# Kernel optimization log

Measured on AMD Instinct MI355X. Metric: run time of the kernel, lower is better.

## Reference

```python
import jax, jax.numpy as jnp
import numpy as np

N = 10000      # nodes (docstring: dense mode intended for <=10k nodes)
D_IN = 64      # in_dim
D_OUT = 64     # out_dim


def setup_inputs() -> dict:
    key = jax.random.key(0)
    kH, kA1, kA2, kA3, kW1, kW2, kW3 = jax.random.split(key, 7)
    H = jax.random.normal(kH, (N, D_IN), dtype=jnp.float32)
    # Dense normalized adjacency per edge type (values in [0,1), as in A_norm)
    A_r1 = jax.random.uniform(kA1, (N, N), dtype=jnp.float32)
    A_r2 = jax.random.uniform(kA2, (N, N), dtype=jnp.float32)
    A_r3 = jax.random.uniform(kA3, (N, N), dtype=jnp.float32)
    # Xavier-uniform init for type-specific linear weights [out_dim, in_dim]
    limit = float(np.sqrt(6.0 / (D_IN + D_OUT)))
    W1 = jax.random.uniform(kW1, (D_OUT, D_IN), dtype=jnp.float32, minval=-limit, maxval=limit)
    W2 = jax.random.uniform(kW2, (D_OUT, D_IN), dtype=jnp.float32, minval=-limit, maxval=limit)
    W3 = jax.random.uniform(kW3, (D_OUT, D_IN), dtype=jnp.float32, minval=-limit, maxval=limit)
    bias = jnp.zeros((D_OUT,), dtype=jnp.float32)
    return {"H": H, "A_r1": A_r1, "A_r2": A_r2, "A_r3": A_r3,
            "W1": W1, "W2": W2, "W3": W3, "bias": bias}


def reference(H, A_r1, A_r2, A_r3, W1, W2, W3, bias):
    # h_v = sum_r W_r @ (sum_u A_r[v,u] * h_u) + b  (no activation in forward)
    out = bias  # broadcasts to [N, D_OUT]
    for A_r, W_r in ((A_r1, W1), (A_r2, W2), (A_r3, W3)):
        msg = A_r @ H                      # [N, D_IN] neighbor aggregation
        out = out + msg @ W_r.T            # [N, D_OUT] type-specific projection
    return out
```

## Files before the change

kernel.cpp:

```cpp
#include <hip/hip_runtime.h>

static constexpr int NN = 10000;
static constexpr int DD = 64;
static constexpr int KP = 10240;
static constexpr int BK = 128;
static constexpr int SPLITS = 4;
static constexpr int KC = KP / SPLITS;
static constexpr int ITERS = KC / BK;
static constexpr int BM = 64;

typedef __attribute__((ext_vector_type(4))) float f32x4;
typedef __attribute__((ext_vector_type(8))) short s16x8;
typedef __attribute__((ext_vector_type(4))) unsigned short u16x4;

__device__ __forceinline__ unsigned short f2bf(float f) {
  unsigned u = __float_as_uint(f);
  return (unsigned short)((u + 0x7fffu + ((u >> 16) & 1u)) >> 16);
}

__device__ __forceinline__ void g2l16(const void* g, void* l) {
  __builtin_amdgcn_global_load_lds((const __attribute__((address_space(1))) unsigned int*)g,
                                   (__attribute__((address_space(3))) unsigned int*)l, 16, 0, 0);
}

__global__ void prep_kernel(const float* __restrict__ H,
                            const float* __restrict__ W1,
                            const float* __restrict__ W2,
                            const float* __restrict__ W3,
                            unsigned short* __restrict__ mt) {
  const int r = blockIdx.y;
  const float* W = (r == 0) ? W1 : (r == 1) ? W2 : W3;
  const int wave = threadIdx.x >> 6;
  const int lane = threadIdx.x & 63;
  f32x4 wr[16];
#pragma unroll
  for (int i = 0; i < 16; ++i) wr[i] = *(const f32x4*)&W[lane * 64 + i * 4];
  unsigned short* orow = mt + ((size_t)r * 64 + lane) * KP;
  const int kbase = blockIdx.x * 128 + wave * 32;
  for (int i = 0; i < 32; ++i) {
    const int k = kbase + i;
    if (k < NN) {
      float s = 0.f;
#pragma unroll
      for (int j = 0; j < 16; ++j) {
        f32x4 h = *(const f32x4*)&H[(size_t)k * 64 + j * 4];
        s += h[0] * wr[j][0] + h[1] * wr[j][1] + h[2] * wr[j][2] + h[3] * wr[j][3];
      }
      orow[k] = f2bf(s);
    } else {
      orow[k] = 0;
    }
  }
}

__global__ void init_out_kernel(const float* __restrict__ bias, float* __restrict__ out) {
  const int i = blockIdx.x * 256 + threadIdx.x;
  if (i < NN * DD) out[i] = bias[i & 63];
}

__global__ __launch_bounds__(256, 2) void gcn_main(const float* __restrict__ A1,
                                                   const float* __restrict__ A2,
                                                   const float* __restrict__ A3,
                                                   const unsigned short* __restrict__ mt,
                                                   float* __restrict__ out) {
  __shared__ __align__(1024) unsigned short mldsM[2][64][128];
  __shared__ __align__(1024) unsigned short mldsA[2][64][128];

  const int r = blockIdx.z;
  const int s = blockIdx.y;
  const float* A = (r == 0) ? A1 : (r == 1) ? A2 : A3;
  const unsigned short* mtr = mt + (size_t)r * 64 * KP;

  const int wave = threadIdx.x >> 6;
  const int lane = threadIdx.x & 63;
  const int l15 = lane & 15;
  const int lhi = lane >> 4;
  const int l31 = lane & 31;
  const int lh5 = lane >> 5;
  const int v0 = blockIdx.x * BM;
  const int k0 = s * KC;

  const float* rowPtr[8];
  int wOff[8];
#pragma unroll
  for (int j = 0; j < 8; ++j) {
    const int rloc = wave * 16 + 2 * j + lh5;
    int vr = v0 + rloc; if (vr > NN - 1) vr = NN - 1;
    rowPtr[j] = A + (size_t)vr * NN;
    wOff[j] = rloc * 256 + (((l31 >> 1) ^ (rloc & 15)) * 16) + (lane & 1) * 8;
  }
  int rOffA[4], rOffM[4][4];
#pragma unroll
  for (int kk = 0; kk < 4; ++kk) {
    rOffA[kk] = (wave * 16 + l15) * 256 + (((kk * 4 + lhi) ^ l15) * 16);
#pragma unroll
    for (int dt = 0; dt < 4; ++dt)
      rOffM[kk][dt] = (dt * 16 + l15) * 256 + (((kk * 4 + lhi) ^ l15) * 16);
  }

  f32x4 acc[4] = {{0.f,0.f,0.f,0.f},{0.f,0.f,0.f,0.f},{0.f,0.f,0.f,0.f},{0.f,0.f,0.f,0.f}};
  f32x4 ar[8];

  auto stageM = [&](int t, int buf) {
    const int kb = k0 + t * BK;
#pragma unroll
    for (int j = 0; j < 4; ++j) {
      const int row16 = 4 * j + (lane >> 4);
      const int rowabs = wave * 16 + row16;
      const unsigned short* src = mtr + (size_t)rowabs * KP + kb + (((lane & 15) ^ row16) << 3);
      g2l16(src, &mldsM[buf][wave * 16 + 4 * j][0]);
    }
  };

  auto issueA = [&](int kb) {
    int koff = kb + l31 * 4;
    if (koff > NN - 4) koff = NN - 4;
    const float* p0 = rowPtr[0] + koff; const float* p1 = rowPtr[1] + koff;
    const float* p2 = rowPtr[2] + koff; const float* p3 = rowPtr[3] + koff;
    const float* p4 = rowPtr[4] + koff; const float* p5 = rowPtr[5] + koff;
    const float* p6 = rowPtr[6] + koff; const float* p7 = rowPtr[7] + koff;
    asm volatile(
      "global_load_dwordx4 %0, %8, off\n\t"
      "global_load_dwordx4 %1, %9, off\n\t"
      "global_load_dwordx4 %2, %10, off\n\t"
      "global_load_dwordx4 %3, %11, off\n\t"
      "global_load_dwordx4 %4, %12, off\n\t"
      "global_load_dwordx4 %5, %13, off\n\t"
      "global_load_dwordx4 %6, %14, off\n\t"
      "global_load_dwordx4 %7, %15, off"
      : "=&v"(ar[0]), "=&v"(ar[1]), "=&v"(ar[2]), "=&v"(ar[3]),
        "=&v"(ar[4]), "=&v"(ar[5]), "=&v"(ar[6]), "=&v"(ar[7])
      : "v"(p0), "v"(p1), "v"(p2), "v"(p3), "v"(p4), "v"(p5), "v"(p6), "v"(p7));
  };

  auto cvtWrite = [&](int buf, int kb) {
    if (kb + BK > NN) {
      if (kb + l31 * 4 > NN - 4) {
#pragma unroll
        for (int j = 0; j < 8; ++j) ar[j] = (f32x4){0.f, 0.f, 0.f, 0.f};
      }
    }
    char* base = (char*)&mldsA[buf][0][0];
#pragma unroll
    for (int j = 0; j < 8; ++j) {
      u16x4 c;
      c[0] = f2bf(ar[j][0]); c[1] = f2bf(ar[j][1]);
      c[2] = f2bf(ar[j][2]); c[3] = f2bf(ar[j][3]);
      *(u16x4*)(base + wOff[j]) = c;
    }
  };

  issueA(k0);
  __builtin_amdgcn_sched_barrier(0);
  stageM(0, 0);
  __builtin_amdgcn_sched_barrier(0);
  asm volatile("s_waitcnt vmcnt(4)");
  __builtin_amdgcn_sched_barrier(0);
  cvtWrite(0, k0);
  __builtin_amdgcn_sched_barrier(0);
  asm volatile("s_waitcnt vmcnt(0)");
  __builtin_amdgcn_sched_barrier(0);
  __builtin_amdgcn_s_barrier();

  for (int t = 0; t < ITERS; ++t) {
    const int buf = t & 1;
    const int tn = (t + 1 < ITERS) ? t + 1 : t;
    const int kbn = k0 + tn * BK;
    issueA(kbn);
    __builtin_amdgcn_sched_barrier(0);
    stageM(tn, buf ^ 1);
    __builtin_amdgcn_sched_barrier(0);
    {
      const char* aBase = (const char*)&mldsA[buf][0][0];
      const char* mBase = (const char*)&mldsM[buf][0][0];
#pragma unroll
      for (int kk = 0; kk < 4; ++kk) {
        s16x8 a = *(const s16x8*)(aBase + rOffA[kk]);
#pragma unroll
        for (int dt = 0; dt < 4; ++dt) {
          s16x8 b = *(const s16x8*)(mBase + rOffM[kk][dt]);
          acc[dt] = __builtin_amdgcn_mfma_f32_16x16x32_bf16(a, b, acc[dt], 0, 0, 0);
        }
      }
    }
    __builtin_amdgcn_sched_barrier(0);
    asm volatile("s_waitcnt vmcnt(4)");
    __builtin_amdgcn_sched_barrier(0);
    cvtWrite(buf ^ 1, kbn);
    __builtin_amdgcn_sched_barrier(0);
    asm volatile("s_waitcnt vmcnt(0)");
    __builtin_amdgcn_sched_barrier(0);
    __builtin_amdgcn_s_barrier();
  }

#pragma unroll
  for (int dt = 0; dt < 4; ++dt) {
    const int d = dt * 16 + l15;
#pragma unroll
    for (int i = 0; i < 4; ++i) {
      const int v = v0 + wave * 16 + lhi * 4 + i;
      if (v < NN) atomicAdd(&out[(size_t)v * DD + d], acc[dt][i]);
    }
  }
}

extern "C" void kernel_launch(void* const* d_in, const int* in_sizes, int n_in,
                              void* d_out, int out_size, void* d_ws, size_t ws_size,
                              hipStream_t stream) {
  const float* H    = (const float*)d_in[0];
  const float* A1   = (const float*)d_in[1];
  const float* A2   = (const float*)d_in[2];
  const float* A3   = (const float*)d_in[3];
  const float* W1   = (const float*)d_in[4];
  const float* W2   = (const float*)d_in[5];
  const float* W3   = (const float*)d_in[6];
  const float* bias = (const float*)d_in[7];
  float* out = (float*)d_out;
  unsigned short* mt = (unsigned short*)d_ws;

  prep_kernel<<<dim3(KP / 128, 3), 256, 0, stream>>>(H, W1, W2, W3, mt);
  init_out_kernel<<<dim3((NN * DD + 255) / 256), 256, 0, stream>>>(bias, out);
  gcn_main<<<dim3((NN + BM - 1) / BM, SPLITS, 3), 256, 0, stream>>>(A1, A2, A3, mt, out);
}
```

Measured before the change: 293.3 us.

## Add alternate direct-to-LDS fp32 A staging path for half the K-splits

Result: no change. 291.3 us (-0.7%).

```diff
diff --git a/kernel.cpp b/kernel.cpp
--- a/kernel.cpp
+++ b/kernel.cpp
@@ -3,10 +3,7 @@
 static constexpr int NN = 10000;
 static constexpr int DD = 64;
 static constexpr int KP = 10240;
-static constexpr int BK = 128;
-static constexpr int SPLITS = 4;
-static constexpr int KC = KP / SPLITS;
-static constexpr int ITERS = KC / BK;
+static constexpr int KC = 2560;
 static constexpr int BM = 64;
 
 typedef __attribute__((ext_vector_type(4))) float f32x4;
@@ -63,11 +60,10 @@
                                                    const float* __restrict__ A3,
                                                    const unsigned short* __restrict__ mt,
                                                    float* __restrict__ out) {
-  __shared__ __align__(1024) unsigned short mldsM[2][64][128];
-  __shared__ __align__(1024) unsigned short mldsA[2][64][128];
+  __shared__ __align__(1024) char smem[65536];
 
   const int r = blockIdx.z;
-  const int s = blockIdx.y;
+  const int sy = blockIdx.y;
   const float* A = (r == 0) ? A1 : (r == 1) ? A2 : A3;
   const unsigned short* mtr = mt + (size_t)r * 64 * KP;
 
@@ -75,122 +71,204 @@
   const int lane = threadIdx.x & 63;
   const int l15 = lane & 15;
   const int lhi = lane >> 4;
-  const int l31 = lane & 31;
-  const int lh5 = lane >> 5;
   const int v0 = blockIdx.x * BM;
-  const int k0 = s * KC;
-
-  const float* rowPtr[8];
-  int wOff[8];
-#pragma unroll
-  for (int j = 0; j < 8; ++j) {
-    const int rloc = wave * 16 + 2 * j + lh5;
-    int vr = v0 + rloc; if (vr > NN - 1) vr = NN - 1;
-    rowPtr[j] = A + (size_t)vr * NN;
-    wOff[j] = rloc * 256 + (((l31 >> 1) ^ (rloc & 15)) * 16) + (lane & 1) * 8;
-  }
-  int rOffA[4], rOffM[4][4];
-#pragma unroll
-  for (int kk = 0; kk < 4; ++kk) {
-    rOffA[kk] = (wave * 16 + l15) * 256 + (((kk * 4 + lhi) ^ l15) * 16);
-#pragma unroll
-    for (int dt = 0; dt < 4; ++dt)
-      rOffM[kk][dt] = (dt * 16 + l15) * 256 + (((kk * 4 + lhi) ^ l15) * 16);
-  }
+  const int k0 = sy * KC;
 
   f32x4 acc[4] = {{0.f,0.f,0.f,0.f},{0.f,0.f,0.f,0.f},{0.f,0.f,0.f,0.f},{0.f,0.f,0.f,0.f}};
-  f32x4 ar[8];
-
-  auto stageM = [&](int t, int buf) {
-    const int kb = k0 + t * BK;
-#pragma unroll
-    for (int j = 0; j < 4; ++j) {
-      const int row16 = 4 * j + (lane >> 4);
-      const int rowabs = wave * 16 + row16;
-      const unsigned short* src = mtr + (size_t)rowabs * KP + kb + (((lane & 15) ^ row16) << 3);
-      g2l16(src, &mldsM[buf][wave * 16 + 4 * j][0]);
-    }
-  };
-
-  auto issueA = [&](int kb) {
-    int koff = kb + l31 * 4;
-    if (koff > NN - 4) koff = NN - 4;
-    const float* p0 = rowPtr[0] + koff; const float* p1 = rowPtr[1] + koff;
-    const float* p2 = rowPtr[2] + koff; const float* p3 = rowPtr[3] + koff;
-    const float* p4 = rowPtr[4] + koff; const float* p5 = rowPtr[5] + koff;
-    const float* p6 = rowPtr[6] + koff; const float* p7 = rowPtr[7] + koff;
-    asm volatile(
-      "global_load_dwordx4 %0, %8, off\n\t"
-      "global_load_dwordx4 %1, %9, off\n\t"
-      "global_load_dwordx4 %2, %10, off\n\t"
-      "global_load_dwordx4 %3, %11, off\n\t"
-      "global_load_dwordx4 %4, %12, off\n\t"
-      "global_load_dwordx4 %5, %13, off\n\t"
-      "global_load_dwordx4 %6, %14, off\n\t"
-      "global_load_dwordx4 %7, %15, off"
-      : "=&v"(ar[0]), "=&v"(ar[1]), "=&v"(ar[2]), "=&v"(ar[3]),
-        "=&v"(ar[4]), "=&v"(ar[5]), "=&v"(ar[6]), "=&v"(ar[7])
-      : "v"(p0), "v"(p1), "v"(p2), "v"(p3), "v"(p4), "v"(p5), "v"(p6), "v"(p7));
-  };
-
-  auto cvtWrite = [&](int buf, int kb) {
-    if (kb + BK > NN) {
-      if (kb + l31 * 4 > NN - 4) {
-#pragma unroll
-        for (int j = 0; j < 8; ++j) ar[j] = (f32x4){0.f, 0.f, 0.f, 0.f};
-      }
-    }
-    char* base = (char*)&mldsA[buf][0][0];
+
+  if (sy < 2) {
+    constexpr int BK = 128, ITERS = 20;
+    auto mldsM = (unsigned short (*)[64][128])(smem);
+    auto mldsA = (unsigned short (*)[64][128])(smem + 32768);
+
+    const int l31 = lane & 31;
+    const int lh5 = lane >> 5;
+
+    const float* rowPtr[8];
+    int wOff[8];
 #pragma unroll
     for (int j = 0; j < 8; ++j) {
-      u16x4 c;
-      c[0] = f2bf(ar[j][0]); c[1] = f2bf(ar[j][1]);
-      c[2] = f2bf(ar[j][2]); c[3] = f2bf(ar[j][3]);
-      *(u16x4*)(base + wOff[j]) = c;
-    }
-  };
-
-  issueA(k0);
-  __builtin_amdgcn_sched_barrier(0);
-  stageM(0, 0);
-  __builtin_amdgcn_sched_barrier(0);
-  asm volatile("s_waitcnt vmcnt(4)");
-  __builtin_amdgcn_sched_barrier(0);
-  cvtWrite(0, k0);
-  __builtin_amdgcn_sched_barrier(0);
-  asm volatile("s_waitcnt vmcnt(0)");
-  __builtin_amdgcn_sched_barrier(0);
-  __builtin_amdgcn_s_barrier();
-
-  for (int t = 0; t < ITERS; ++t) {
-    const int buf = t & 1;
-    const int tn = (t + 1 < ITERS) ? t + 1 : t;
-    const int kbn = k0 + tn * BK;
-    issueA(kbn);
-    __builtin_amdgcn_sched_barrier(0);
-    stageM(tn, buf ^ 1);
-    __builtin_amdgcn_sched_barrier(0);
-    {
-      const char* aBase = (const char*)&mldsA[buf][0][0];
-      const char* mBase = (const char*)&mldsM[buf][0][0];
-#pragma unroll
-      for (int kk = 0; kk < 4; ++kk) {
-        s16x8 a = *(const s16x8*)(aBase + rOffA[kk]);
+      const int rloc = wave * 16 + 2 * j + lh5;
+      int vr = v0 + rloc; if (vr > NN - 1) vr = NN - 1;
+      rowPtr[j] = A + (size_t)vr * NN;
+      wOff[j] = rloc * 256 + (((l31 >> 1) ^ (rloc & 15)) * 16) + (lane & 1) * 8;
+    }
+    int rOffA[4], rOffM[4][4];
+#pragma unroll
+    for (int kk = 0; kk < 4; ++kk) {
+      rOffA[kk] = (wave * 16 + l15) * 256 + (((kk * 4 + lhi) ^ l15) * 16);
+#pragma unroll
+      for (int dt = 0; dt < 4; ++dt)
+        rOffM[kk][dt] = (dt * 16 + l15) * 256 + (((kk * 4 + lhi) ^ l15) * 16);
+    }
+
+    f32x4 ar[8];
+
+    auto stageM = [&](int t, int buf) {
+      const int kb = k0 + t * BK;
+#pragma unroll
+      for (int j = 0; j < 4; ++j) {
+        const int row16 = 4 * j + (lane >> 4);
+        const int rowabs = wave * 16 + row16;
+        const unsigned short* src = mtr + (size_t)rowabs * KP + kb + (((lane & 15) ^ row16) << 3);
+        g2l16(src, &mldsM[buf][wave * 16 + 4 * j][0]);
+      }
+    };
+    auto issueA = [&](int kb) {
+      int koff = kb + l31 * 4;
+      if (koff > NN - 4) koff = NN - 4;
+      const float* p0 = rowPtr[0] + koff; const float* p1 = rowPtr[1] + koff;
+      const float* p2 = rowPtr[2] + koff; const float* p3 = rowPtr[3] + koff;
+      const float* p4 = rowPtr[4] + koff; const float* p5 = rowPtr[5] + koff;
+      const float* p6 = rowPtr[6] + koff; const float* p7 = rowPtr[7] + koff;
+      asm volatile(
+        "global_load_dwordx4 %0, %8, off\n\t"
+        "global_load_dwordx4 %1, %9, off\n\t"
+        "global_load_dwordx4 %2, %10, off\n\t"
+        "global_load_dwordx4 %3, %11, off\n\t"
+        "global_load_dwordx4 %4, %12, off\n\t"
+        "global_load_dwordx4 %5, %13, off\n\t"
+        "global_load_dwordx4 %6, %14, off\n\t"
+        "global_load_dwordx4 %7, %15, off"
+        : "=&v"(ar[0]), "=&v"(ar[1]), "=&v"(ar[2]), "=&v"(ar[3]),
+          "=&v"(ar[4]), "=&v"(ar[5]), "=&v"(ar[6]), "=&v"(ar[7])
+        : "v"(p0), "v"(p1), "v"(p2), "v"(p3), "v"(p4), "v"(p5), "v"(p6), "v"(p7));
+    };
+    auto cvtWrite = [&](int buf, int kb) {
+      if (kb + BK > NN) {
+        if (kb + l31 * 4 > NN - 4) {
+#pragma unroll
+          for (int j = 0; j < 8; ++j) ar[j] = (f32x4){0.f, 0.f, 0.f, 0.f};
+        }
+      }
+      char* base = (char*)&mldsA[0][0][0] + buf * 32768 / 2;
+#pragma unroll
+      for (int j = 0; j < 8; ++j) {
+        u16x4 c;
+        c[0] = f2bf(ar[j][0]); c[1] = f2bf(ar[j][1]);
+        c[2] = f2bf(ar[j][2]); c[3] = f2bf(ar[j][3]);
+        *(u16x4*)(base + wOff[j]) = c;
+      }
+    };
+
+    issueA(k0);
+    __builtin_amdgcn_sched_barrier(0);
+    stageM(0, 0);
+    __builtin_amdgcn_sched_barrier(0);
+    asm volatile("s_waitcnt vmcnt(4)");
+    __builtin_amdgcn_sched_barrier(0);
+    cvtWrite(0, k0);
+    __builtin_amdgcn_sched_barrier(0);
+    asm volatile("s_waitcnt vmcnt(0)");
+    __builtin_amdgcn_sched_barrier(0);
+    __builtin_amdgcn_s_barrier();
+
+    for (int t = 0; t < ITERS; ++t) {
+      const int buf = t & 1;
+      const int tn = (t + 1 < ITERS) ? t + 1 : t;
+      const int kbn = k0 + tn * BK;
+      issueA(kbn);
+      __builtin_amdgcn_sched_barrier(0);
+      stageM(tn, buf ^ 1);
+      __builtin_amdgcn_sched_barrier(0);
+      {
+        const char* aBase = (const char*)&mldsA[0][0][0] + buf * 16384;
+        const char* mBase = (const char*)&mldsM[0][0][0] + buf * 16384;
+#pragma unroll
+        for (int kk = 0; kk < 4; ++kk) {
+          s16x8 a = *(const s16x8*)(aBase + rOffA[kk]);
+#pragma unroll
+          for (int dt = 0; dt < 4; ++dt) {
+            s16x8 b = *(const s16x8*)(mBase + rOffM[kk][dt]);
+            acc[dt] = __builtin_amdgcn_mfma_f32_16x16x32_bf16(a, b, acc[dt], 0, 0, 0);
+          }
+        }
+      }
+      __builtin_amdgcn_sched_barrier(0);
+      asm volatile("s_waitcnt vmcnt(4)");
+      __builtin_amdgcn_sched_barrier(0);
+      cvtWrite(buf ^ 1, kbn);
+      __builtin_amdgcn_sched_barrier(0);
+      asm volatile("s_waitcnt vmcnt(0)");
+      __builtin_amdgcn_sched_barrier(0);
+      __builtin_amdgcn_s_barrier();
+    }
+  } else {
+    constexpr int BK = 64, ITERS = 40;
+    auto alds  = (float (*)[64][64])(smem);
+    auto mlds2 = (unsigned short (*)[64][64])(smem + 32768);
+
+    auto stageA = [&](int t, int buf) {
+      const int kb = k0 + t * BK;
+#pragma unroll
+      for (int j = 0; j < 4; ++j) {
+        const int row16 = 4 * j + lhi;
+        int vr = v0 + wave * 16 + row16;
+        if (vr > NN - 1) vr = NN - 1;
+        int colf = kb + ((l15 ^ row16) << 2);
+        if (colf > NN - 4) colf = NN - 4;
+        g2l16(A + (size_t)vr * NN + colf, &alds[buf][wave * 16 + 4 * j][0]);
+      }
+    };
+    auto stageM = [&](int t, int buf) {
+      const int kb = k0 + t * BK;
+#pragma unroll
+      for (int j = 0; j < 2; ++j) {
+        const int row16 = 8 * j + (lane >> 3);
+        const int gsm = (lane & 7) ^ (lane >> 3);
+        g2l16(mtr + (size_t)(wave * 16 + row16) * KP + kb + gsm * 8,
+              &mlds2[buf][wave * 16 + 8 * j][0]);
+      }
+    };
+    auto cvtA = [&](const f32x4& x, const f32x4& y) -> s16x8 {
+      s16x8 v;
+      v[0] = (short)f2bf(x[0]); v[1] = (short)f2bf(x[1]);
+      v[2] = (short)f2bf(x[2]); v[3] = (short)f2bf(x[3]);
+      v[4] = (short)f2bf(y[0]); v[5] = (short)f2bf(y[1]);
+      v[6] = (short)f2bf(y[2]); v[7] = (short)f2bf(y[3]);
+      return v;
+    };
+    auto compute = [&](int t, int buf) {
+#pragma unroll
+      for (int kk = 0; kk < 2; ++kk) {
+        const int g0 = kk * 8 + lhi * 2;
+        const int s0 = g0 ^ l15;
+        const f32x4 x = *(const f32x4*)&alds[buf][wave * 16 + l15][s0 * 4];
+        const f32x4 y = *(const f32x4*)&alds[buf][wave * 16 + l15][(s0 ^ 1) * 4];
+        s16x8 a = cvtA(x, y);
 #pragma unroll
         for (int dt = 0; dt < 4; ++dt) {
-          s16x8 b = *(const s16x8*)(mBase + rOffM[kk][dt]);
+          const int sm = (kk * 4 + lhi) ^ (l15 & 7);
+          s16x8 b = *(const s16x8*)&mlds2[buf][dt * 16 + l15][sm * 8];
           acc[dt] = __builtin_amdgcn_mfma_f32_16x16x32_bf16(a, b, acc[dt], 0, 0, 0);
         }
       }
-    }
-    __builtin_amdgcn_sched_barrier(0);
-    asm volatile("s_waitcnt vmcnt(4)");
-    __builtin_amdgcn_sched_barrier(0);
-    cvtWrite(buf ^ 1, kbn);
-    __builtin_amdgcn_sched_barrier(0);
+    };
+
+    stageA(0, 0); stageM(0, 0);
+    stageA(1, 1); stageM(1, 1);
+    __builtin_amdgcn_sched_barrier(0);
+    asm volatile("s_waitcnt vmcnt(6)");
+    __builtin_amdgcn_sched_barrier(0);
+    __builtin_amdgcn_s_barrier();
+    __builtin_amdgcn_sched_barrier(0);
+
+    for (int t = 0; t < ITERS - 1; ++t) {
+      const int buf = t & 1;
+      compute(t, buf);
+      __builtin_amdgcn_sched_barrier(0);
+      __builtin_amdgcn_s_barrier();
+      __builtin_amdgcn_sched_barrier(0);
+      const int tc = (t + 2 < ITERS) ? t + 2 : ITERS - 1;
+      stageA(tc, buf); stageM(tc, buf);
+      __builtin_amdgcn_sched_barrier(0);
+      asm volatile("s_waitcnt vmcnt(6)");
+      __builtin_amdgcn_sched_barrier(0);
+      __builtin_amdgcn_s_barrier();
+      __builtin_amdgcn_sched_barrier(0);
+    }
+    compute(ITERS - 1, (ITERS - 1) & 1);
     asm volatile("s_waitcnt vmcnt(0)");
-    __builtin_amdgcn_sched_barrier(0);
-    __builtin_amdgcn_s_barrier();
   }
 
 #pragma unroll
@@ -220,5 +298,5 @@
 
   prep_kernel<<<dim3(KP / 128, 3), 256, 0, stream>>>(H, W1, W2, W3, mt);
   init_out_kernel<<<dim3((NN * DD + 255) / 256), 256, 0, stream>>>(bias, out);
-  gcn_main<<<dim3((NN + BM - 1) / BM, SPLITS, 3), 256, 0, stream>>>(A1, A2, A3, mt, out);
-}
+  gcn_main<<<dim3((NN + BM - 1) / BM, 4, 3), 256, 0, stream>>>(A1, A2, A3, mt, out);
+}
```
